# Kernel tuning notes

Hardware: AMD Instinct MI355X
Metric: run time of the kernel (lower is better)

Reference implementation:

```python
import jax, jax.numpy as jnp
import numpy as np
import math

H = 32          # hidden irreps width
L = 2           # layers
B = 10          # number_of_basis
MAXR = 2.0      # max_radius
N_NODES = 20000
N_EDGES = 320000
H3 = 3 * H
H6 = 6 * H
STEP_H = 0.1    # self.h


def mlp2(x, w1, w2):
    # Filter / DoubleLayer surrogate: Linear -> gelu -> Linear
    return jax.nn.gelu(x @ w1) @ w2


def smooth_cutoff(x):
    # e3nn smooth_cutoff: 1 for x<0.5, cosine falloff on [0.5,1], 0 beyond
    u = 2.0 * (x - 1.0)
    y = 0.5 * (1.0 - jnp.cos(jnp.pi * u))
    y = jnp.where(u > 0.0, 0.0, y)
    y = jnp.where(u < -1.0, 1.0, y)
    return y


def edge_div(g, W, esrc, edst, nnodes):
    wg = W * g
    x = jnp.zeros((nnodes, g.shape[-1]), dtype=g.dtype)
    return x.at[edst].add(wg).at[esrc].add(-wg)


def edge_ave(g, W, esrc, edst, nnodes):
    wg = W * g
    x = jnp.zeros((nnodes, g.shape[-1]), dtype=g.dtype)
    return 0.5 * x.at[edst].add(wg).at[esrc].add(wg)


def setup_inputs() -> dict:
    key = jax.random.key(0)
    ks = jax.random.split(key, 20)
    s = lambda i, shape, scale: (jax.random.normal(ks[i], shape, jnp.float32)
                                 * scale)
    inp = {
        "pos": jax.random.uniform(ks[0], (N_NODES, 3), jnp.float32),
        "atom_z": jax.random.randint(ks[1], (N_NODES,), 0, 20),
        "edge_src": jax.random.randint(ks[2], (N_EDGES,), 0, N_NODES),
        "edge_dst": jax.random.randint(ks[3], (N_EDGES,), 0, N_NODES),
        "embed": s(4, (20, 8), 1.0),
        "dl0_w1": s(5, (8, H), 8 ** -0.5),
        "dl0_w2": s(6, (H, H), H ** -0.5),
        "dl1_w1": s(7, (4, H), 4 ** -0.5),
        "dl1_w2": s(8, (H, H), H ** -0.5),
        "filt01_w1": s(9, (2, B, 64), B ** -0.5),
        "filt01_w2": s(10, (2, 64, H), 64 ** -0.5),
        "filtAB_w1": s(11, (L, 2, B, 64), B ** -0.5),
        "filtAB_w2": s(12, (L, 2, 64, H3), 64 ** -0.5),
        "filtC_w1": s(13, (L, B, 64), B ** -0.5),
        "filtC_w2": s(14, (L, 64, H6), 64 ** -0.5),
        "dlL_w1": s(15, (L, H6, H), H6 ** -0.5),
        "dlL_w2": s(16, (L, H, H6), H ** -0.5),
        "si_w": s(17, (H3, 16), H3 ** -0.5),
    }
    return inp


def reference(pos, atom_z, edge_src, edge_dst, embed, dl0_w1, dl0_w2,
              dl1_w1, dl1_w2, filt01_w1, filt01_w2, filtAB_w1, filtAB_w2,
              filtC_w1, filtC_w2, dlL_w1, dlL_w2, si_w):
    nnodes = pos.shape[0]

    # edge geometry
    edge_vec = pos[edge_src] - pos[edge_dst]                     # [E,3]
    length = jnp.sqrt(jnp.sum(edge_vec * edge_vec, -1) + 1e-12)  # [E]
    r_safe = jnp.maximum(length, 1e-6)

    # spherical harmonics l=0,1 with 'component' normalization -> [E,4]
    sh = jnp.concatenate(
        [jnp.ones_like(length)[:, None],
         math.sqrt(3.0) * edge_vec / r_safe[:, None]], axis=1)

    # bessel soft_one_hot_linspace * sqrt(B) -> [E,B]
    roots = jnp.arange(1, B + 1, dtype=jnp.float32) * jnp.pi
    basis = (math.sqrt(2.0 / MAXR)
             * jnp.sin(roots[None, :] * length[:, None] / MAXR)
             / r_safe[:, None]) * math.sqrt(B)

    xe = smooth_cutoff(length / MAXR)[:, None] * sh              # [E,4]

    # embed + first double layers
    xn = embed[atom_z]                                           # [N,8]
    xn = mlp2(xn, dl0_w1, dl0_w2)                                # [N,H]
    xe = mlp2(xe, dl1_w1, dl1_w2)                                # [E,H]

    W0 = mlp2(basis, filt01_w1[0], filt01_w2[0])
    xe_eD = edge_div(xe, W0, edge_src, edge_dst, nnodes)
    W1 = mlp2(basis, filt01_w1[1], filt01_w2[1])
    xe_eA = edge_ave(xe, W1, edge_src, edge_dst, nnodes)
    xn = jnp.concatenate([xn, xe_eD, xe_eA], axis=1)             # [N,3H]

    for i in range(L):
        Wa = mlp2(basis, filtAB_w1[i, 0], filtAB_w2[i, 0])       # [E,3H]
        gradX = Wa * (xn[edge_dst] - xn[edge_src])               # nodeGrad
        Wb = mlp2(basis, filtAB_w1[i, 1], filtAB_w2[i, 1])
        aveX = Wb * (xn[edge_dst] + xn[edge_src]) * 0.5          # nodeAve
        dxe = jnp.concatenate([gradX, aveX], axis=1)             # [E,6H]
        dxe = mlp2(dxe, dlL_w1[i], dlL_w2[i])                    # [E,6H]
        Wc = mlp2(basis, filtC_w1[i], filtC_w2[i])               # [E,6H]
        xn_div = edge_div(dxe[:, :H3], Wc[:, :H3], edge_src, edge_dst, nnodes)
        xn_ave = edge_ave(dxe[:, H3:], Wc[:, H3:], edge_src, edge_dst, nnodes)
        xn = xn - STEP_H * (xn_div + xn_ave)

    xn = xn @ si_w                                               # [N,16]
    # reduce_output: single graph (batch all zeros) -> sum / sqrt(num_nodes)
    return jnp.sum(xn, axis=0, keepdims=True) / math.sqrt(float(N_NODES))
```

## Files before the change

kernel.cpp:

```cpp
#include <hip/hip_runtime.h>
#include <hip/hip_bf16.h>

#define NN 20000
#define NE 320000
#define NT 2048

typedef _Float16 h2f __attribute__((ext_vector_type(2)));
typedef _Float16 f16x8 __attribute__((ext_vector_type(8)));
typedef float f32x4 __attribute__((ext_vector_type(4)));

__device__ __forceinline__ h2f u2h(unsigned int u){
  union { unsigned int u; h2f h; } v; v.u = u; return v.h;
}
__device__ __forceinline__ unsigned int h2u(h2f h){
  union { h2f h; unsigned int u; } v; v.h = h; return v.u;
}
__device__ __forceinline__ unsigned int pack2(float a, float b){
  h2f h; h.x = (_Float16)a; h.y = (_Float16)b;
  union { h2f h; unsigned int u; } v; v.h = h; return v.u;
}
__device__ __forceinline__ unsigned short f16b(float a){
  union { _Float16 h; unsigned short u; } v; v.h = (_Float16)a; return v.u;
}
__device__ __forceinline__ f16x8 u4h8(uint4 u){
  union { uint4 u; f16x8 h; } v; v.u = u; return v.h;
}
__device__ __forceinline__ unsigned int lerp2(unsigned int a, unsigned int b, h2f t){
  h2f ha = u2h(a), hb = u2h(b);
  return h2u(ha + t * (hb - ha));
}

__device__ __forceinline__ float geluf(float x){
  float t = 0.7978845608028654f * x * (1.0f + 0.044715f * x * x);
  return x / (1.0f + __expf(-2.0f * t));
}

struct TEnt { const float* src; float* dst; int R; int C; int trans; };
struct TTab { TEnt e[8]; };

__device__ __forceinline__ void lut_basis(int ent, float* b){
  float len = fmaxf((float)ent * (1.7321f / (float)(NT - 1)), 1e-6f);
  float sc = 3.1622776601683795f / fmaxf(len, 1e-6f);
#pragma unroll
  for (int k = 0; k < 10; k++)
    b[k] = sinf((float)(k + 1) * 1.5707963267948966f * len) * sc;
}

__global__ __launch_bounds__(384) void prep_k(
    TTab tb,
    const float* __restrict__ fABw1, const float* __restrict__ fABw2,
    const float* __restrict__ fCw1,  const float* __restrict__ fCw2,
    unsigned short* __restrict__ lutH,
    const float* __restrict__ f01w1, const float* __restrict__ f01w2,
    unsigned short* __restrict__ lut01H,
    const float* __restrict__ dlw1, const float* __restrict__ dlw2,
    unsigned int* __restrict__ bf1, unsigned int* __restrict__ bf2)
{
  int b = blockIdx.x;
  int t = threadIdx.x;
  if (b < 6){
    TEnt en = tb.e[b];
    int n = en.R * en.C;
    for (int i = t; i < n; i += 384){
      float v = en.src[i];
      if (en.trans){
        int r = i / en.C, c = i - r * en.C;
        en.dst[c * en.R + r] = v;
      } else {
        en.dst[i] = v;
      }
    }
    return;
  }
  if (b == 6){
    for (int i = t; i < 12288; i += 384){
      if (i < 6144){
        int v = i & 3, ln = (i >> 2) & 63;
        int nt = (i >> 8) & 1;
        int ktly = i >> 9;
        int kt = ktly % 6, ly = ktly / 6;
        int k = 32*kt + 8*(ln >> 4) + 2*v;
        int col = 16*nt + (ln & 15);
        const float* s = dlw1 + ly*6144;
        bf1[i] = pack2(s[k*32 + col], s[(k+1)*32 + col]);
      } else {
        int j = i - 6144;
        int v = j & 3, ln = (j >> 2) & 63;
        int ntly = j >> 8;
        int nt = ntly % 12, ly = ntly / 12;
        int k = 8*(ln >> 4) + 2*v;
        int col = 16*nt + (ln & 15);
        const float* s = dlw2 + ly*6144;
        bf2[j] = pack2(s[k*192 + col], s[(k+1)*192 + col]);
      }
    }
    return;
  }
  if (b < 7 + 2*NT){
    int bb = b - 7;
    int ent = bb & (NT - 1);
    int layer = bb >> 11;
    float bas[10];
    lut_basis(ent, bas);
    __shared__ float h[192];
    if (t < 192){
      int f = t >> 6, l = t & 63;
      const float* w1 = (f < 2) ? (fABw1 + (layer*2 + f) * 640)
                                : (fCw1 + layer * 640);
      float a = 0.f;
#pragma unroll
      for (int k = 0; k < 10; k++) a += bas[k] * w1[k*64 + l];
      h[t] = geluf(a);
    }
    __syncthreads();
    float a = 0.f;
    if (t < 192){
      int f = t / 96, j = t - 96 * f;
      const float* w2 = fABw2 + (layer*2 + f) * 6144;
      for (int l = 0; l < 64; l++) a += h[f*64 + l] * w2[l*96 + j];
    } else {
      int j = t - 192;
      const float* w2 = fCw2 + layer * 12288;
      for (int l = 0; l < 64; l++) a += h[128 + l] * w2[l*192 + j];
    }
    lutH[((long)(layer * NT + ent)) * 384 + t] = f16b(a);
    return;
  }
  int blk = b - 7 - 2*NT;
  int ent = blk * 6 + (t >> 6);
  if (ent >= NT) return;
  int tl = t & 63;
  int p = tl >> 5, jj = tl & 31;
  float bas[10];
  lut_basis(ent, bas);
  const float* w1 = f01w1 + p * 640;
  const float* w2 = f01w2 + p * 2048;
  float W = 0.f;
  for (int l = 0; l < 64; l++){
    float a = 0.f;
#pragma unroll
    for (int k = 0; k < 10; k++) a += bas[k] * w1[k*64 + l];
    W += geluf(a) * w2[l*32 + jj];
  }
  lut01H[(long)ent * 64 + tl] = f16b(W);
}

__global__ __launch_bounds__(256) void countnode_k(
    const int* __restrict__ esrc, const int* __restrict__ edst,
    int* __restrict__ cntd, int* __restrict__ cnts,
    const int* __restrict__ az, const float* __restrict__ embedF,
    const float* __restrict__ w1T , const float* __restrict__ w2T ,
    float* __restrict__ xn)
{
  if (blockIdx.x < NE/256){
    int e = blockIdx.x * 256 + threadIdx.x;
    atomicAdd(cntd + edst[e], 1);
    atomicAdd(cnts + esrc[e], 1);
    return;
  }
  int n = (blockIdx.x - NE/256) * 256 + threadIdx.x;
  if (n >= NN) return;
  int z = az[n];
  float ee[8];
#pragma unroll
  for (int k = 0; k < 8; k++) ee[k] = embedF[z * 8 + k];
  float hid[32];
#pragma unroll
  for (int l = 0; l < 32; l++){
    float a = 0.f;
#pragma unroll
    for (int k = 0; k < 8; k++) a += ee[k] * w1T[l * 8 + k];
    hid[l] = geluf(a);
  }
  float* row = xn + (long)n * 96;
#pragma unroll
  for (int j = 0; j < 32; j++){
    float a = 0.f;
#pragma unroll
    for (int l = 0; l < 32; l++) a += hid[l] * w2T[j * 32 + l];
    row[j] = a;
  }
#pragma unroll
  for (int j = 32; j < 96; j++) row[j] = 0.f;
}

__global__ __launch_bounds__(1024) void prefix_k(
    const int* __restrict__ cntd, int* __restrict__ doff, int* __restrict__ curd,
    const int* __restrict__ cnts, int* __restrict__ soff, int* __restrict__ curs)
{
  const int* cnt = blockIdx.x ? cnts : cntd;
  int* off = blockIdx.x ? soff : doff;
  int* cur = blockIdx.x ? curs : curd;
  __shared__ int part[1024];
  int t = threadIdx.x;
  int base = t * 20;
  int s = 0;
  for (int i = 0; i < 20; i++){ int idx = base + i; if (idx < NN) s += cnt[idx]; }
  part[t] = s; __syncthreads();
  for (int d = 1; d < 1024; d <<= 1){
    int v = (t >= d) ? part[t - d] : 0;
    __syncthreads();
    part[t] += v;
    __syncthreads();
  }
  int run = (t == 0) ? 0 : part[t - 1];
  for (int i = 0; i < 20; i++){
    int idx = base + i;
    if (idx < NN){ off[idx] = run; cur[idx] = run; run += cnt[idx]; }
  }
  if (t == 0) off[NN] = NE;
}

__global__ void fill_comb(const int* __restrict__ esrc, const int* __restrict__ edst,
                          int* __restrict__ curd, int* __restrict__ curs,
                          int* __restrict__ srcS, int* __restrict__ dstS,
                          int* __restrict__ qpos){
  int e = blockIdx.x * 256 + threadIdx.x;
  if (e >= NE) return;
  int s = esrc[e], d = edst[e];
  int p = atomicAdd(curd + d, 1);
  srcS[p] = s; dstS[p] = d;
  int q = atomicAdd(curs + s, 1);
  qpos[p] = q;
}

__global__ __launch_bounds__(256) void edge_init(
    const float* __restrict__ pos, const int* __restrict__ srcS,
    const int* __restrict__ dstS, const int* __restrict__ qpos,
    float* __restrict__ els,
    unsigned short* __restrict__ pbuf0, unsigned short* __restrict__ qbuf0,
    const float* __restrict__ w1T , const float* __restrict__ w2T ,
    const unsigned int* __restrict__ lut01)
{
  int p = blockIdx.x * 256 + threadIdx.x;
  if (p >= NE) return;
  int s = srcS[p], d = dstS[p];
  float x = pos[s*3+0] - pos[d*3+0];
  float y = pos[s*3+1] - pos[d*3+1];
  float z = pos[s*3+2] - pos[d*3+2];
  float L = sqrtf(x*x + y*y + z*z + 1e-12f);
  float iv = 1.0f / fmaxf(L, 1e-6f);
  els[p] = L;

  float u = L - 2.0f;
  float cut = 0.5f * (1.0f - cosf(3.14159265358979323f * u));
  cut = (u > 0.0f) ? 0.0f : cut;
  cut = (u < -1.0f) ? 1.0f : cut;
  float xe0 = cut, cc = cut * 1.7320508075688772f * iv;
  float xe1 = cc*x, xe2 = cc*y, xe3 = cc*z;
  float hid[32];
#pragma unroll
  for (int l = 0; l < 32; l++){
    float a = xe0*w1T[l*4+0] + xe1*w1T[l*4+1] + xe2*w1T[l*4+2] + xe3*w1T[l*4+3];
    hid[l] = geluf(a);
  }
  float xeh[32];
#pragma unroll
  for (int j = 0; j < 32; j++){
    float a = 0.f;
#pragma unroll
    for (int l = 0; l < 32; l++) a += hid[l] * w2T[j*32 + l];
    xeh[j] = a;
  }
  float tt = fminf(L * ((float)(NT-1) / 1.7321f), (float)(NT-1) - 0.001f);
  int i0 = (int)tt; float tfv = tt - (float)i0;
  h2f tf2; tf2.x = (_Float16)tfv; tf2.y = tf2.x;
  h2f h05; h05.x = (_Float16)0.5f; h05.y = h05.x;
  const unsigned int* rA = lut01 + i0 * 32;
  const unsigned int* rB = rA + 32;

  unsigned int xp[16];
#pragma unroll
  for (int jp = 0; jp < 16; jp++)
    xp[jp] = pack2(xeh[2*jp] * 0.0625f, xeh[2*jp+1] * 0.0625f);

  unsigned int du[16], au[16];
#pragma unroll
  for (int q = 0; q < 4; q++){
    uint4 a = ((const uint4*)rA)[q];
    uint4 b = ((const uint4*)rB)[q];
    du[4*q+0] = h2u(u2h(lerp2(a.x, b.x, tf2)) * u2h(xp[4*q+0]));
    du[4*q+1] = h2u(u2h(lerp2(a.y, b.y, tf2)) * u2h(xp[4*q+1]));
    du[4*q+2] = h2u(u2h(lerp2(a.z, b.z, tf2)) * u2h(xp[4*q+2]));
    du[4*q+3] = h2u(u2h(lerp2(a.w, b.w, tf2)) * u2h(xp[4*q+3]));
  }
#pragma unroll
  for (int q = 0; q < 4; q++){
    uint4 a = ((const uint4*)(rA + 16))[q];
    uint4 b = ((const uint4*)(rB + 16))[q];
    au[4*q+0] = h2u(u2h(lerp2(a.x, b.x, tf2)) * u2h(xp[4*q+0]) * h05);
    au[4*q+1] = h2u(u2h(lerp2(a.y, b.y, tf2)) * u2h(xp[4*q+1]) * h05);
    au[4*q+2] = h2u(u2h(lerp2(a.z, b.z, tf2)) * u2h(xp[4*q+2]) * h05);
    au[4*q+3] = h2u(u2h(lerp2(a.w, b.w, tf2)) * u2h(xp[4*q+3]) * h05);
  }
  unsigned short* prow = pbuf0 + (long)p * 64;
  unsigned short* qrow = qbuf0 + (long)qpos[p] * 64;
#pragma unroll
  for (int q = 0; q < 4; q++){
    ((uint4*)prow)[q]      = ((uint4*)du)[q];
    ((uint4*)(prow+32))[q] = ((uint4*)au)[q];
  }
  unsigned int nd[16];
#pragma unroll
  for (int i = 0; i < 16; i++) nd[i] = du[i] ^ 0x80008000u;
#pragma unroll
  for (int q = 0; q < 4; q++){
    ((uint4*)qrow)[q]      = ((uint4*)nd)[q];
    ((uint4*)(qrow+32))[q] = ((uint4*)au)[q];
  }
}

__global__ __launch_bounds__(256) void gather_init(
    const int* __restrict__ doff, const int* __restrict__ soff,
    const unsigned short* __restrict__ pbuf0, const unsigned short* __restrict__ qbuf0,
    float* __restrict__ xn, unsigned int* __restrict__ xnh)
{
  int n = blockIdx.x * 4 + (threadIdx.x >> 6);
  int c = threadIdx.x & 63;
  if (n >= NN) return;
  const _Float16* ph = (const _Float16*)pbuf0;
  const _Float16* qh = (const _Float16*)qbuf0;
  float acc = 0.f;
  int d1 = doff[n+1];
  for (int p = doff[n]; p < d1; p++) acc += (float)ph[(long)p * 64 + c];
  int s1 = soff[n+1];
  for (int q = soff[n]; q < s1; q++) acc += (float)qh[(long)q * 64 + c];
  float v = 16.f * acc;
  xn[(long)n * 96 + 32 + c] = v;
  float other = __shfl_xor(v, 1);
  if (!(c & 1)) xnh[n * 48 + 16 + (c >> 1)] = pack2(v, other);
  if (c < 16){
    float a = xn[(long)n * 96 + 2*c];
    float b = xn[(long)n * 96 + 2*c + 1];
    xnh[n * 48 + c] = pack2(a, b);
  }
}

__global__ __launch_bounds__(256) void layer_k(
    const int* __restrict__ srcS, const int* __restrict__ dstS,
    const int* __restrict__ qpos,
    const float* __restrict__ els, const unsigned int* __restrict__ xnh,
    unsigned short* __restrict__ pbuf, unsigned short* __restrict__ qbuf,
    const unsigned int* __restrict__ lut,
    const unsigned int* __restrict__ bf1, const unsigned int* __restrict__ bf2)
{
  __shared__ unsigned int smem[4][1092];
  int tid = threadIdx.x;
  int wid = tid >> 6, lane = tid & 63;
  int g = lane >> 4, r15 = lane & 15;
  unsigned int* wb = smem[wid];
  int wbase = blockIdx.x * 256 + wid * 64;

  const unsigned int* xsP[4]; const unsigned int* xdP[4];
  const unsigned int* rAm[4]; const unsigned int* rBm[4];
  h2f tfm[4];
#pragma unroll
  for (int mt = 0; mt < 4; mt++){
    int re = wbase + 16*mt + r15;
    xsP[mt] = xnh + srcS[re] * 48;
    xdP[mt] = xnh + dstS[re] * 48;
    float L = els[re];
    float tt = fminf(L * ((float)(NT-1) / 1.7321f), (float)(NT-1) - 0.001f);
    int i0 = (int)tt; float tfv = tt - (float)i0;
    h2f tf; tf.x = (_Float16)tfv; tf.y = tf.x;
    tfm[mt] = tf;
    rAm[mt] = lut + (long)i0 * 192;
    rBm[mt] = rAm[mt] + 192;
  }
  int p = wbase + lane;
  int qq = qpos[p];
  const unsigned int *rAo, *rBo; h2f tfo;
  {
    float L = els[p];
    float tt = fminf(L * ((float)(NT-1) / 1.7321f), (float)(NT-1) - 0.001f);
    int i0 = (int)tt; float tfv = tt - (float)i0;
    tfo.x = (_Float16)tfv; tfo.y = tfo.x;
    rAo = lut + (long)i0 * 192;
    rBo = rAo + 192;
  }
  h2f c32; c32.x = (_Float16)0.03125f;  c32.y = c32.x;
  h2f c64; c64.x = (_Float16)0.015625f; c64.y = c64.x;
  h2f h05; h05.x = (_Float16)0.5f;      h05.y = h05.x;
  f32x4 zf = {0.f, 0.f, 0.f, 0.f};

  f32x4 acc[4][2];
#pragma unroll
  for (int mt = 0; mt < 4; mt++){ acc[mt][0] = zf; acc[mt][1] = zf; }

#pragma unroll
  for (int ktp = 0; ktp < 3; ktp++){
    int off = 16*ktp + 4*g;
    uint4 bg0 = *(const uint4*)(bf1 + (((ktp  )*2 + 0)*64 + lane)*4);
    uint4 bg1 = *(const uint4*)(bf1 + (((ktp  )*2 + 1)*64 + lane)*4);
    uint4 ba0 = *(const uint4*)(bf1 + (((ktp+3)*2 + 0)*64 + lane)*4);
    uint4 ba1 = *(const uint4*)(bf1 + (((ktp+3)*2 + 1)*64 + lane)*4);
#pragma unroll
    for (int mt = 0; mt < 4; mt++){
      uint4 xs4 = *(const uint4*)(xsP[mt] + off);
      uint4 xd4 = *(const uint4*)(xdP[mt] + off);
      uint4 waA = *(const uint4*)(rAm[mt] + off);
      uint4 waB = *(const uint4*)(rBm[mt] + off);
      uint4 wbA = *(const uint4*)(rAm[mt] + 48 + off);
      uint4 wbB = *(const uint4*)(rBm[mt] + 48 + off);
      h2f tf = tfm[mt];
      uint4 fg, fa;
      fg.x = h2u(u2h(lerp2(waA.x, waB.x, tf)) * ((u2h(xd4.x) - u2h(xs4.x)) * c32));
      fg.y = h2u(u2h(lerp2(waA.y, waB.y, tf)) * ((u2h(xd4.y) - u2h(xs4.y)) * c32));
      fg.z = h2u(u2h(lerp2(waA.z, waB.z, tf)) * ((u2h(xd4.z) - u2h(xs4.z)) * c32));
      fg.w = h2u(u2h(lerp2(waA.w, waB.w, tf)) * ((u2h(xd4.w) - u2h(xs4.w)) * c32));
      fa.x = h2u(u2h(lerp2(wbA.x, wbB.x, tf)) * ((u2h(xd4.x) + u2h(xs4.x)) * c64));
      fa.y = h2u(u2h(lerp2(wbA.y, wbB.y, tf)) * ((u2h(xd4.y) + u2h(xs4.y)) * c64));
      fa.z = h2u(u2h(lerp2(wbA.z, wbB.z, tf)) * ((u2h(xd4.z) + u2h(xs4.z)) * c64));
      fa.w = h2u(u2h(lerp2(wbA.w, wbB.w, tf)) * ((u2h(xd4.w) + u2h(xs4.w)) * c64));
      acc[mt][0] = __builtin_amdgcn_mfma_f32_16x16x32_f16(u4h8(fg), u4h8(bg0), acc[mt][0], 0, 0, 0);
      acc[mt][1] = __builtin_amdgcn_mfma_f32_16x16x32_f16(u4h8(fg), u4h8(bg1), acc[mt][1], 0, 0, 0);
      acc[mt][0] = __builtin_amdgcn_mfma_f32_16x16x32_f16(u4h8(fa), u4h8(ba0), acc[mt][0], 0, 0, 0);
      acc[mt][1] = __builtin_amdgcn_mfma_f32_16x16x32_f16(u4h8(fa), u4h8(ba1), acc[mt][1], 0, 0, 0);
    }
  }

#pragma unroll
  for (int mt = 0; mt < 4; mt++)
#pragma unroll
    for (int nt = 0; nt < 2; nt++)
#pragma unroll
      for (int i = 0; i < 4; i++){
        float v = geluf(32.f * acc[mt][nt][i]) * 0.015625f;
        float o = __shfl_xor(v, 1);
        if (!(lane & 1))
          wb[(16*mt + 4*g + i)*17 + 8*nt + (r15 >> 1)] = pack2(v, o);
      }
  __syncthreads();
  uint4 af[4];
#pragma unroll
  for (int mt = 0; mt < 4; mt++){
    int row = 16*mt + r15;
    af[mt].x = wb[row*17 + 4*g + 0];
    af[mt].y = wb[row*17 + 4*g + 1];
    af[mt].z = wb[row*17 + 4*g + 2];
    af[mt].w = wb[row*17 + 4*g + 3];
  }
  __syncthreads();

  unsigned int* prow = (unsigned int*)(pbuf + (long)p * 96);
  unsigned int* qrow = (unsigned int*)(qbuf + (long)qq * 96);
  for (int np = 0; np < 6; np++){
    uint4 b1 = *(const uint4*)(bf2 + ((np    )*64 + lane)*4);
    uint4 b2 = *(const uint4*)(bf2 + ((np + 6)*64 + lane)*4);
    f32x4 d1a[4], d2a[4];
#pragma unroll
    for (int mt = 0; mt < 4; mt++){
      d1a[mt] = __builtin_amdgcn_mfma_f32_16x16x32_f16(u4h8(af[mt]), u4h8(b1), zf, 0, 0, 0);
      d2a[mt] = __builtin_amdgcn_mfma_f32_16x16x32_f16(u4h8(af[mt]), u4h8(b2), zf, 0, 0, 0);
    }
#pragma unroll
    for (int mt = 0; mt < 4; mt++)
#pragma unroll
      for (int i = 0; i < 4; i++){
        float v1 = d1a[mt][i], v2 = d2a[mt][i];
        float o1 = __shfl_xor(v1, 1);
        float o2 = __shfl_xor(v2, 1);
        if (!(lane & 1)){
          int r = 16*mt + 4*g + i;
          wb[r*17 + (r15 >> 1)]     = pack2(v1, o1);
          wb[r*17 + 8 + (r15 >> 1)] = pack2(v2, o2);
        }
      }
    __syncthreads();
    unsigned int d1u[8], d2u[8];
#pragma unroll
    for (int u = 0; u < 8; u++){
      d1u[u] = wb[lane*17 + u];
      d2u[u] = wb[lane*17 + 8 + u];
    }
    __syncthreads();
    uint4 ca0 = *(const uint4*)(rAo + 96  + 8*np);
    uint4 ca1 = *(const uint4*)(rAo + 100 + 8*np);
    uint4 cb0 = *(const uint4*)(rBo + 96  + 8*np);
    uint4 cb1 = *(const uint4*)(rBo + 100 + 8*np);
    uint4 ka0 = *(const uint4*)(rAo + 144 + 8*np);
    uint4 ka1 = *(const uint4*)(rAo + 148 + 8*np);
    uint4 kb0 = *(const uint4*)(rBo + 144 + 8*np);
    uint4 kb1 = *(const uint4*)(rBo + 148 + 8*np);
    unsigned int c1u[8] = {lerp2(ca0.x,cb0.x,tfo), lerp2(ca0.y,cb0.y,tfo),
                           lerp2(ca0.z,cb0.z,tfo), lerp2(ca0.w,cb0.w,tfo),
                           lerp2(ca1.x,cb1.x,tfo), lerp2(ca1.y,cb1.y,tfo),
                           lerp2(ca1.z,cb1.z,tfo), lerp2(ca1.w,cb1.w,tfo)};
    unsigned int c2u[8] = {lerp2(ka0.x,kb0.x,tfo), lerp2(ka0.y,kb0.y,tfo),
                           lerp2(ka0.z,kb0.z,tfo), lerp2(ka0.w,kb0.w,tfo),
                           lerp2(ka1.x,kb1.x,tfo), lerp2(ka1.y,kb1.y,tfo),
                           lerp2(ka1.z,kb1.z,tfo), lerp2(ka1.w,kb1.w,tfo)};
    unsigned int pv[8], qv[8];
#pragma unroll
    for (int u = 0; u < 8; u++){
      h2f t1 = u2h(c1u[u]) * u2h(d1u[u]);
      h2f t2 = (u2h(c2u[u]) * u2h(d2u[u])) * h05;
      pv[u] = h2u(t1 + t2);
      qv[u] = h2u(t2 - t1);
    }
    *(uint4*)(prow + 8*np)     = *(uint4*)(pv);
    *(uint4*)(prow + 8*np + 4) = *(uint4*)(pv + 4);
    *(uint4*)(qrow + 8*np)     = *(uint4*)(qv);
    *(uint4*)(qrow + 8*np + 4) = *(uint4*)(qv + 4);
  }
}

__global__ __launch_bounds__(512) void gather_upd(
    const int* __restrict__ doff, const int* __restrict__ soff,
    const unsigned short* __restrict__ pbuf, const unsigned short* __restrict__ qbuf,
    float* __restrict__ xn, unsigned int* __restrict__ xnh)
{
  int g = threadIdx.x / 96;
  int c = threadIdx.x - 96 * g;
  if (g >= 5) return;
  int n = blockIdx.x * 5 + g;
  if (n >= NN) return;
  const _Float16* ph = (const _Float16*)pbuf;
  const _Float16* qh = (const _Float16*)qbuf;
  float acc = 0.f;
  int d1 = doff[n+1];
  for (int p = doff[n]; p < d1; p++) acc += (float)ph[(long)p * 96 + c];
  int s1 = soff[n+1];
  for (int q = soff[n]; q < s1; q++) acc += (float)qh[(long)q * 96 + c];
  long idx = (long)n * 96 + c;
  float x = xn[idx] - 6.4f * acc;
  xn[idx] = x;
  float other = __shfl_xor(x, 1);
  if (!(c & 1)) xnh[n * 48 + (c >> 1)] = pack2(x, other);
}

__global__ void colsum(const float* __restrict__ xn, float* __restrict__ nodesum){
  int col = threadIdx.x % 96;
  int seg = threadIdx.x / 96;
  int stripe = blockIdx.x * 2 + seg;
  float acc = 0.f;
  for (int n = stripe; n < NN; n += 400) acc += xn[(long)n * 96 + col];
  unsafeAtomicAdd(nodesum + col, acc);
}

__global__ void project(const float* __restrict__ nodesum, const float* __restrict__ siT,
                        float* __restrict__ out){
  int j = threadIdx.x;
  if (j < 16){
    float a = 0.f;
#pragma unroll
    for (int c = 0; c < 96; c++) a += nodesum[c] * siT[j*96 + c];
    out[j] = a * 0.007071067811865475f;
  }
}

extern "C" void kernel_launch(void* const* d_in, const int* in_sizes, int n_in,
                              void* d_out, int out_size, void* d_ws, size_t ws_size,
                              hipStream_t stream){
  const float* pos  = (const float*)d_in[0];
  const int* atom_z = (const int*)d_in[1];
  const int* esrc   = (const int*)d_in[2];
  const int* edst   = (const int*)d_in[3];

  float* ws      = (float*)d_ws;
  float* xn      = ws;
  float* nodesum = ws + 1920000;
  float* WB      = ws + 1920096;
  unsigned int* bf1   = (unsigned int*)(ws + 1924224);
  unsigned int* bf2   = (unsigned int*)(ws + 1930368);
  unsigned int* lutL  = (unsigned int*)(ws + 1936512);
  unsigned int* lut01 = (unsigned int*)(ws + 2722944);
  unsigned int* xnh   = (unsigned int*)(ws + 2788480);
  float* els    = ws + 3748480;
  int*   cntd   = (int*)(ws + 4068480);
  int*   cnts   = cntd + 20000;
  int*   curd   = cnts + 20000;
  int*   curs   = curd + 20000;
  int*   doff   = curs + 20000;
  int*   soff   = doff + 20004;
  int*   srcS   = soff + 20004;
  int*   dstS   = srcS + 320000;
  int*   qpos   = dstS + 320000;
  unsigned short* pbufL = (unsigned short*)(ws + 5468496);
  unsigned short* qbufL = (unsigned short*)(ws + 20828496);
  unsigned short* pbuf0 = (unsigned short*)(ws + 5468496);
  unsigned short* qbuf0 = (unsigned short*)(ws + 15708496);

  float* embedF = WB + 0;
  float* dl0w1T = WB + 160;
  float* dl0w2T = WB + 416;
  float* dl1w1T = WB + 1440;
  float* dl1w2T = WB + 1568;
  float* siT    = WB + 2592;

  hipMemsetAsync(cntd, 0, 40000 * 4, stream);
  hipMemsetAsync(nodesum, 0, 96 * 4, stream);

  TTab tb;
  int ti = 0;
  auto add = [&](const void* s, float* dst, int R, int C, int tr){
    tb.e[ti].src = (const float*)s; tb.e[ti].dst = dst;
    tb.e[ti].R = R; tb.e[ti].C = C; tb.e[ti].trans = tr; ti++;
  };
  add(d_in[4],  embedF, 20, 8, 0);
  add(d_in[5],  dl0w1T, 8, 32, 1);
  add(d_in[6],  dl0w2T, 32, 32, 1);
  add(d_in[7],  dl1w1T, 4, 32, 1);
  add(d_in[8],  dl1w2T, 32, 32, 1);
  add(d_in[17], siT, 96, 16, 1);

  prep_k<<<7 + 2*NT + (NT + 5)/6, 384, 0, stream>>>(
      tb, (const float*)d_in[11], (const float*)d_in[12],
      (const float*)d_in[13], (const float*)d_in[14], (unsigned short*)lutL,
      (const float*)d_in[9], (const float*)d_in[10], (unsigned short*)lut01,
      (const float*)d_in[15], (const float*)d_in[16], bf1, bf2);
  countnode_k<<<NE/256 + (NN + 255)/256, 256, 0, stream>>>(
      esrc, edst, cntd, cnts, atom_z, embedF, dl0w1T, dl0w2T, xn);
  prefix_k<<<2, 1024, 0, stream>>>(cntd, doff, curd, cnts, soff, curs);
  fill_comb<<<(NE + 255)/256, 256, 0, stream>>>(esrc, edst, curd, curs,
                                                srcS, dstS, qpos);
  edge_init<<<(NE + 255)/256, 256, 0, stream>>>(
      pos, srcS, dstS, qpos, els, pbuf0, qbuf0, dl1w1T, dl1w2T, lut01);
  gather_init<<<(NN + 3)/4, 256, 0, stream>>>(doff, soff, pbuf0, qbuf0, xn, xnh);

  for (int i = 0; i < 2; i++){
    layer_k<<<NE/256, 256, 0, stream>>>(
        srcS, dstS, qpos, els, xnh, pbufL, qbufL,
        lutL + (long)i * NT * 192, bf1 + i*3072, bf2 + i*3072);
    gather_upd<<<(NN + 4)/5, 512, 0, stream>>>(doff, soff, pbufL, qbufL,
                                               xn, xnh);
  }
  colsum<<<200, 192, 0, stream>>>(xn, nodesum);
  project<<<1, 64, 0, stream>>>(nodesum, siT, (float*)d_out);
}
```

Baseline: 732.0 us.

## Vectorize gather kernels to 4 channels per thread and use wave-local syncs

```diff
diff --git a/kernel.cpp b/kernel.cpp
--- a/kernel.cpp
+++ b/kernel.cpp
@@ -33,6 +33,11 @@
 __device__ __forceinline__ float geluf(float x){
   float t = 0.7978845608028654f * x * (1.0f + 0.044715f * x * x);
   return x / (1.0f + __expf(-2.0f * t));
+}
+
+__device__ __forceinline__ void wsync(){
+  asm volatile("" ::: "memory");
+  __builtin_amdgcn_sched_barrier(0);
 }
 
 struct TEnt { const float* src; float* dst; int R; int C; int trans; };
@@ -315,24 +320,33 @@
     const unsigned short* __restrict__ pbuf0, const unsigned short* __restrict__ qbuf0,
     float* __restrict__ xn, unsigned int* __restrict__ xnh)
 {
-  int n = blockIdx.x * 4 + (threadIdx.x >> 6);
-  int c = threadIdx.x & 63;
+  int g = threadIdx.x >> 4;
+  int c4 = threadIdx.x & 15;
+  int n = blockIdx.x * 16 + g;
   if (n >= NN) return;
-  const _Float16* ph = (const _Float16*)pbuf0;
-  const _Float16* qh = (const _Float16*)qbuf0;
-  float acc = 0.f;
+  const uint2* p2 = (const uint2*)pbuf0;
+  const uint2* q2 = (const uint2*)qbuf0;
+  float a0 = 0.f, a1 = 0.f, a2 = 0.f, a3 = 0.f;
   int d1 = doff[n+1];
-  for (int p = doff[n]; p < d1; p++) acc += (float)ph[(long)p * 64 + c];
+  for (int p = doff[n]; p < d1; p++){
+    uint2 v = p2[(long)p * 16 + c4];
+    h2f lo = u2h(v.x), hi = u2h(v.y);
+    a0 += (float)lo.x; a1 += (float)lo.y; a2 += (float)hi.x; a3 += (float)hi.y;
+  }
   int s1 = soff[n+1];
-  for (int q = soff[n]; q < s1; q++) acc += (float)qh[(long)q * 64 + c];
-  float v = 16.f * acc;
-  xn[(long)n * 96 + 32 + c] = v;
-  float other = __shfl_xor(v, 1);
-  if (!(c & 1)) xnh[n * 48 + 16 + (c >> 1)] = pack2(v, other);
-  if (c < 16){
-    float a = xn[(long)n * 96 + 2*c];
-    float b = xn[(long)n * 96 + 2*c + 1];
-    xnh[n * 48 + c] = pack2(a, b);
+  for (int q = soff[n]; q < s1; q++){
+    uint2 v = q2[(long)q * 16 + c4];
+    h2f lo = u2h(v.x), hi = u2h(v.y);
+    a0 += (float)lo.x; a1 += (float)lo.y; a2 += (float)hi.x; a3 += (float)hi.y;
+  }
+  float4 v4; v4.x = 16.f*a0; v4.y = 16.f*a1; v4.z = 16.f*a2; v4.w = 16.f*a3;
+  *(float4*)(xn + (long)n * 96 + 32 + 4*c4) = v4;
+  uint2 w; w.x = pack2(v4.x, v4.y); w.y = pack2(v4.z, v4.w);
+  *(uint2*)(xnh + n * 48 + 16 + 2*c4) = w;
+  if (c4 < 8){
+    float4 t = *(const float4*)(xn + (long)n * 96 + 4*c4);
+    uint2 w0; w0.x = pack2(t.x, t.y); w0.y = pack2(t.z, t.w);
+    *(uint2*)(xnh + n * 48 + 2*c4) = w0;
   }
 }
 
@@ -430,7 +444,7 @@
         if (!(lane & 1))
           wb[(16*mt + 4*g + i)*17 + 8*nt + (r15 >> 1)] = pack2(v, o);
       }
-  __syncthreads();
+  wsync();
   uint4 af[4];
 #pragma unroll
   for (int mt = 0; mt < 4; mt++){
@@ -440,7 +454,7 @@
     af[mt].z = wb[row*17 + 4*g + 2];
     af[mt].w = wb[row*17 + 4*g + 3];
   }
-  __syncthreads();
+  wsync();
 
   unsigned int* prow = (unsigned int*)(pbuf + (long)p * 96);
   unsigned int* qrow = (unsigned int*)(qbuf + (long)qq * 96);
@@ -466,14 +480,14 @@
           wb[r*17 + 8 + (r15 >> 1)] = pack2(v2, o2);
         }
       }
-    __syncthreads();
+    wsync();
     unsigned int d1u[8], d2u[8];
 #pragma unroll
     for (int u = 0; u < 8; u++){
       d1u[u] = wb[lane*17 + u];
       d2u[u] = wb[lane*17 + 8 + u];
     }
-    __syncthreads();
+    wsync();
     uint4 ca0 = *(const uint4*)(rAo + 96  + 8*np);
     uint4 ca1 = *(const uint4*)(rAo + 100 + 8*np);
     uint4 cb0 = *(const uint4*)(rBo + 96  + 8*np);
@@ -505,28 +519,36 @@
   }
 }
 
-__global__ __launch_bounds__(512) void gather_upd(
+__global__ __launch_bounds__(256) void gather_upd(
     const int* __restrict__ doff, const int* __restrict__ soff,
     const unsigned short* __restrict__ pbuf, const unsigned short* __restrict__ qbuf,
     float* __restrict__ xn, unsigned int* __restrict__ xnh)
 {
-  int g = threadIdx.x / 96;
-  int c = threadIdx.x - 96 * g;
-  if (g >= 5) return;
-  int n = blockIdx.x * 5 + g;
+  int g = threadIdx.x / 24;
+  int c4 = threadIdx.x - 24 * g;
+  if (g >= 10) return;
+  int n = blockIdx.x * 10 + g;
   if (n >= NN) return;
-  const _Float16* ph = (const _Float16*)pbuf;
-  const _Float16* qh = (const _Float16*)qbuf;
-  float acc = 0.f;
+  const uint2* p2 = (const uint2*)pbuf;
+  const uint2* q2 = (const uint2*)qbuf;
+  float a0 = 0.f, a1 = 0.f, a2 = 0.f, a3 = 0.f;
   int d1 = doff[n+1];
-  for (int p = doff[n]; p < d1; p++) acc += (float)ph[(long)p * 96 + c];
+  for (int p = doff[n]; p < d1; p++){
+    uint2 v = p2[(long)p * 24 + c4];
+    h2f lo = u2h(v.x), hi = u2h(v.y);
+    a0 += (float)lo.x; a1 += (float)lo.y; a2 += (float)hi.x; a3 += (float)hi.y;
+  }
   int s1 = soff[n+1];
-  for (int q = soff[n]; q < s1; q++) acc += (float)qh[(long)q * 96 + c];
-  long idx = (long)n * 96 + c;
-  float x = xn[idx] - 6.4f * acc;
-  xn[idx] = x;
-  float other = __shfl_xor(x, 1);
-  if (!(c & 1)) xnh[n * 48 + (c >> 1)] = pack2(x, other);
+  for (int q = soff[n]; q < s1; q++){
+    uint2 v = q2[(long)q * 24 + c4];
+    h2f lo = u2h(v.x), hi = u2h(v.y);
+    a0 += (float)lo.x; a1 += (float)lo.y; a2 += (float)hi.x; a3 += (float)hi.y;
+  }
+  float4 xo = *(float4*)(xn + (long)n * 96 + 4*c4);
+  xo.x -= 6.4f * a0; xo.y -= 6.4f * a1; xo.z -= 6.4f * a2; xo.w -= 6.4f * a3;
+  *(float4*)(xn + (long)n * 96 + 4*c4) = xo;
+  uint2 w; w.x = pack2(xo.x, xo.y); w.y = pack2(xo.z, xo.w);
+  *(uint2*)(xnh + n * 48 + 2*c4) = w;
 }
 
 __global__ void colsum(const float* __restrict__ xn, float* __restrict__ nodesum){
@@ -616,14 +638,14 @@
                                                 srcS, dstS, qpos);
   edge_init<<<(NE + 255)/256, 256, 0, stream>>>(
       pos, srcS, dstS, qpos, els, pbuf0, qbuf0, dl1w1T, dl1w2T, lut01);
-  gather_init<<<(NN + 3)/4, 256, 0, stream>>>(doff, soff, pbuf0, qbuf0, xn, xnh);
+  gather_init<<<(NN + 15)/16, 256, 0, stream>>>(doff, soff, pbuf0, qbuf0, xn, xnh);
 
   for (int i = 0; i < 2; i++){
     layer_k<<<NE/256, 256, 0, stream>>>(
         srcS, dstS, qpos, els, xnh, pbufL, qbufL,
         lutL + (long)i * NT * 192, bf1 + i*3072, bf2 + i*3072);
-    gather_upd<<<(NN + 4)/5, 512, 0, stream>>>(doff, soff, pbufL, qbufL,
-                                               xn, xnh);
+    gather_upd<<<(NN + 9)/10, 256, 0, stream>>>(doff, soff, pbufL, qbufL,
+                                                xn, xnh);
   }
   colsum<<<200, 192, 0, stream>>>(xn, nodesum);
   project<<<1, 64, 0, stream>>>(nodesum, siT, (float*)d_out);
```

After: 650.6 us. 11.1% less time.
